# Kernel tuning notes

Measured on AMD Instinct MI355X. Metric: run time of the kernel, lower is better.

## Reference

```python
import jax, jax.numpy as jnp
import numpy as np

NUM_USERS = 100000
NUM_ITEMS = 50000
EMBED_DIM = 64
N_LAYERS = 3
NNZ = 4800000
BATCH = 16384
N_NODES = NUM_USERS + NUM_ITEMS


def setup_inputs() -> dict:
    key = jax.random.key(0)
    k1, k2, k3, k4, k5, k6, k7 = jax.random.split(key, 7)
    users = jax.random.randint(k1, (BATCH,), 0, NUM_USERS, dtype=jnp.int64 if jax.config.jax_enable_x64 else jnp.int32)
    items = jax.random.randint(k2, (BATCH,), 0, NUM_ITEMS, dtype=jnp.int64 if jax.config.jax_enable_x64 else jnp.int32)
    adj_rows = jax.random.randint(k3, (NNZ,), 0, N_NODES, dtype=jnp.int32)
    adj_cols = jax.random.randint(k4, (NNZ,), 0, N_NODES, dtype=jnp.int32)
    adj_vals = jax.random.uniform(k5, (NNZ,), dtype=jnp.float32)
    user_emb = jax.random.normal(k6, (NUM_USERS, EMBED_DIM), dtype=jnp.float32)
    item_emb = jax.random.normal(k7, (NUM_ITEMS, EMBED_DIM), dtype=jnp.float32)
    return {"users": users, "items": items, "adj_rows": adj_rows,
            "adj_cols": adj_cols, "adj_vals": adj_vals,
            "user_emb": user_emb, "item_emb": item_emb}


def _spmm(rows, cols, vals, x):
    # y = A @ x for COO sparse A: gather source rows, scale, scatter-add to dest
    return jax.ops.segment_sum(vals[:, None] * x[cols], rows, num_segments=N_NODES)


def reference(users, items, adj_rows, adj_cols, adj_vals, user_emb, item_emb):
    ego = jnp.concatenate([user_emb, item_emb], axis=0)  # [N_NODES, D]
    acc = ego
    cur = ego
    for _ in range(N_LAYERS):
        cur = _spmm(adj_rows, adj_cols, adj_vals, cur)
        acc = acc + cur
    mean_emb = acc / jnp.float32(N_LAYERS + 1)
    user_final = mean_emb[:NUM_USERS]
    item_final = mean_emb[NUM_USERS:]
    u = user_final[users]  # [B, D]
    i = item_final[items]  # [B, D]
    return jnp.sum(u * i, axis=-1)  # [B]
```

## Files before the change

### kernel.cpp

```cpp
#include <hip/hip_runtime.h>
#include <hip/hip_bf16.h>

#define NUM_USERS 100000
#define NUM_ITEMS 50000
#define EMBED_DIM 64
#define N_NODES   150000
#define ROW_SHIFT 9
#define ROWS_PER_BUCKET 512
#define B_BUCKETS ((N_NODES + ROWS_PER_BUCKET - 1) / ROWS_PER_BUCKET)
#define NBP 512
#define BIN_CHUNK 2048
#define COL_MASK 0x3FFFF

typedef unsigned short ushort_t;
typedef unsigned int uint_t;

__device__ __forceinline__ float bf16_to_f32(ushort_t u) {
    return __uint_as_float(((unsigned)u) << 16);
}
__device__ __forceinline__ ushort_t f32_to_bf16(float f) {
    return __builtin_bit_cast(ushort_t, __float2bfloat16(f));
}
__device__ __forceinline__ float bflo(uint_t r) {
    return __uint_as_float(r << 16);
}
__device__ __forceinline__ float bfhi(uint_t r) {
    return __uint_as_float(r & 0xffff0000u);
}

__global__ void __launch_bounds__(512) k_bucket_hist(const int* __restrict__ rows,
                                                     int* __restrict__ bhist, int nnz) {
    __shared__ int lh[NBP];
    int t = threadIdx.x;
    lh[t] = 0;
    __syncthreads();
    int base = blockIdx.x * (512 * 32);
#pragma unroll
    for (int k = 0; k < 32; k++) {
        int idx = base + k * 512 + t;
        if (idx < nnz) atomicAdd(&lh[rows[idx] >> ROW_SHIFT], 1);
    }
    __syncthreads();
    if (t < B_BUCKETS && lh[t] > 0) atomicAdd(&bhist[t], lh[t]);
}

__global__ void __launch_bounds__(512) k_bucket_scan(const int* __restrict__ bhist,
                                                     int* __restrict__ bucket_off,
                                                     int* __restrict__ bucket_cursor,
                                                     int* __restrict__ offs, int nnz) {
    __shared__ int lds[NBP];
    int t = threadIdx.x;
    int v = (t < B_BUCKETS) ? bhist[t] : 0;
    lds[t] = v;
    __syncthreads();
    for (int d = 1; d < NBP; d <<= 1) {
        int y = (t >= d) ? lds[t - d] : 0;
        __syncthreads();
        lds[t] += y;
        __syncthreads();
    }
    int excl = lds[t] - v;
    if (t < B_BUCKETS) {
        bucket_off[t] = excl;
        bucket_cursor[t] = excl;
    }
    if (t == 0) {
        bucket_off[B_BUCKETS] = nnz;
        offs[N_NODES] = nnz;
    }
}

__global__ void __launch_bounds__(512) k_bin(const int* __restrict__ rows,
                                             const int* __restrict__ cols,
                                             const float* __restrict__ vals,
                                             int* __restrict__ bucket_cursor,
                                             int2* __restrict__ staging, int nnz) {
    __shared__ int  ccnt[NBP];
    __shared__ int  cpos[NBP];
    __shared__ int  gdst[NBP];
    __shared__ int2 entries[BIN_CHUNK];
    __shared__ ushort_t ebuck[BIN_CHUNK];

    int t = threadIdx.x;
    int base = blockIdx.x * BIN_CHUNK;
    ccnt[t] = 0;
    __syncthreads();

    int myrow[BIN_CHUNK / 512];
#pragma unroll
    for (int k = 0; k < BIN_CHUNK / 512; k++) {
        int idx = base + k * 512 + t;
        int r = (idx < nnz) ? rows[idx] : -1;
        myrow[k] = r;
        if (r >= 0) atomicAdd(&ccnt[r >> ROW_SHIFT], 1);
    }
    __syncthreads();

    int c = ccnt[t];
    cpos[t] = c;
    __syncthreads();
    for (int d = 1; d < NBP; d <<= 1) {
        int y = (t >= d) ? cpos[t - d] : 0;
        __syncthreads();
        cpos[t] += y;
        __syncthreads();
    }
    int total = cpos[NBP - 1];
    int excl = cpos[t] - c;
    __syncthreads();
    cpos[t] = excl;
    __syncthreads();

#pragma unroll
    for (int k = 0; k < BIN_CHUNK / 512; k++) {
        int r = myrow[k];
        if (r >= 0) {
            int idx = base + k * 512 + t;
            int b = r >> ROW_SHIFT;
            int lrow = r & (ROWS_PER_BUCKET - 1);
            int slot = atomicAdd(&cpos[b], 1);
            entries[slot] = make_int2(cols[idx] | (lrow << 18), __float_as_int(vals[idx]));
            ebuck[slot] = (ushort_t)b;
        }
    }
    __syncthreads();

    if (t < B_BUCKETS && ccnt[t] > 0) {
        int g = atomicAdd(&bucket_cursor[t], ccnt[t]);
        gdst[t] = g - (cpos[t] - ccnt[t]);
    }
    __syncthreads();

    for (int i = t; i < total; i += 512) {
        staging[gdst[ebuck[i]] + i] = entries[i];
    }
}

__global__ void __launch_bounds__(512) k_scatter2(const int2* __restrict__ staging,
                                                  const int* __restrict__ bucket_off,
                                                  int* __restrict__ offs,
                                                  int2* __restrict__ cv) {
    __shared__ int rc[ROWS_PER_BUCKET];
    int b = blockIdx.x;
    int t = threadIdx.x;
    int beg = bucket_off[b], end = bucket_off[b + 1];
    int row0 = b << ROW_SHIFT;

    rc[t] = 0;
    __syncthreads();
    for (int i = beg + t; i < end; i += 512)
        atomicAdd(&rc[staging[i].x >> 18], 1);
    __syncthreads();

    int c = rc[t];
    for (int d = 1; d < ROWS_PER_BUCKET; d <<= 1) {
        int y = (t >= d) ? rc[t - d] : 0;
        __syncthreads();
        rc[t] += y;
        __syncthreads();
    }
    int excl = rc[t] - c;
    int row = row0 + t;
    if (row < N_NODES) offs[row] = beg + excl;
    __syncthreads();
    rc[t] = excl;
    __syncthreads();

    for (int i = beg + t; i < end; i += 512) {
        int2 e = staging[i];
        int pos = beg + atomicAdd(&rc[e.x >> 18], 1);
        cv[pos] = make_int2(e.x & COL_MASK, e.y);
    }
}

__global__ void k_convert(const float* __restrict__ ue, const float* __restrict__ ie,
                          ushort_t* __restrict__ xb) {
    int i = blockIdx.x * blockDim.x + threadIdx.x;
    const int n4 = (N_NODES * EMBED_DIM) / 4;
    if (i >= n4) return;
    const int usplit = (NUM_USERS * EMBED_DIM) / 4;
    float4 f = (i < usplit) ? ((const float4*)ue)[i] : ((const float4*)ie)[i - usplit];
    ushort4 o;
    o.x = f32_to_bf16(f.x);
    o.y = f32_to_bf16(f.y);
    o.z = f32_to_bf16(f.z);
    o.w = f32_to_bf16(f.w);
    ((ushort4*)xb)[i] = o;
}

__device__ __forceinline__ float2 spmm_row(int beg, int end, int hl, bool hi_half,
                                           const int2* __restrict__ cv,
                                           const ushort_t* __restrict__ xb) {
    const uint_t* __restrict__ xw = (const uint_t*)xb;
    float ax = 0.f, ay = 0.f;
    int e = beg;
    int npair = (end - beg) >> 1;
    int ng = npair >> 3;

    if (ng > 0) {
        uint_t r0[8], r1[8];
        float ve0[8], vo0[8], ve1[8], vo1[8];
#pragma unroll
        for (int j = 0; j < 8; j++) {
            int2 c0 = cv[e + 2 * j];
            int2 c1 = cv[e + 2 * j + 1];
            int ce = __builtin_amdgcn_readfirstlane(c0.x);
            int co = __builtin_amdgcn_readfirstlane(c1.x);
            ve0[j] = __int_as_float(__builtin_amdgcn_readfirstlane(c0.y));
            vo0[j] = __int_as_float(__builtin_amdgcn_readfirstlane(c1.y));
            int col = hi_half ? co : ce;
            r0[j] = xw[(size_t)col * 32 + hl];
        }
        e += 16;
#pragma unroll 1
        for (int g = 1; g < ng; g++) {
#pragma unroll
            for (int j = 0; j < 8; j++) {
                int2 c0 = cv[e + 2 * j];
                int2 c1 = cv[e + 2 * j + 1];
                int ce = __builtin_amdgcn_readfirstlane(c0.x);
                int co = __builtin_amdgcn_readfirstlane(c1.x);
                ve1[j] = __int_as_float(__builtin_amdgcn_readfirstlane(c0.y));
                vo1[j] = __int_as_float(__builtin_amdgcn_readfirstlane(c1.y));
                int col = hi_half ? co : ce;
                r1[j] = xw[(size_t)col * 32 + hl];
            }
            e += 16;
#pragma unroll
            for (int j = 0; j < 8; j++) {
                float v = hi_half ? vo0[j] : ve0[j];
                ax += v * bflo(r0[j]);
                ay += v * bfhi(r0[j]);
            }
#pragma unroll
            for (int j = 0; j < 8; j++) {
                r0[j] = r1[j]; ve0[j] = ve1[j]; vo0[j] = vo1[j];
            }
        }
#pragma unroll
        for (int j = 0; j < 8; j++) {
            float v = hi_half ? vo0[j] : ve0[j];
            ax += v * bflo(r0[j]);
            ay += v * bfhi(r0[j]);
        }
    }
#pragma unroll 1
    for (; e + 2 <= end; e += 2) {
        int2 c0 = cv[e];
        int2 c1 = cv[e + 1];
        int ce = __builtin_amdgcn_readfirstlane(c0.x);
        int co = __builtin_amdgcn_readfirstlane(c1.x);
        float ve = __int_as_float(__builtin_amdgcn_readfirstlane(c0.y));
        float vo = __int_as_float(__builtin_amdgcn_readfirstlane(c1.y));
        int col = hi_half ? co : ce;
        uint_t r = xw[(size_t)col * 32 + hl];
        float v = hi_half ? vo : ve;
        ax += v * bflo(r);
        ay += v * bfhi(r);
    }
    if (e < end) {
        int2 c = cv[e];
        int ce = __builtin_amdgcn_readfirstlane(c.x);
        float ve = __int_as_float(__builtin_amdgcn_readfirstlane(c.y));
        uint_t r = xw[(size_t)ce * 32 + hl];
        float v = hi_half ? 0.f : ve;
        ax += v * bflo(r);
        ay += v * bfhi(r);
    }
    ax += __shfl_xor(ax, 32, 64);
    ay += __shfl_xor(ay, 32, 64);
    return make_float2(ax, ay);
}

__global__ void k_spmm(const int* __restrict__ offs, const int2* __restrict__ cv,
                       const ushort_t* __restrict__ xb, ushort_t* __restrict__ out) {
    int row = (blockIdx.x * blockDim.x + threadIdx.x) >> 6;
    int lane = threadIdx.x & 63;
    if (row >= N_NODES) return;
    int hl = lane & 31;
    bool hi_half = lane >= 32;
    row = __builtin_amdgcn_readfirstlane(row);
    int beg = __builtin_amdgcn_readfirstlane(offs[row]);
    int end = __builtin_amdgcn_readfirstlane(offs[row + 1]);
    float2 a = spmm_row(beg, end, hl, hi_half, cv, xb);
    if (!hi_half) {
        uint_t packed = ((uint_t)f32_to_bf16(a.y) << 16) | (uint_t)f32_to_bf16(a.x);
        ((uint_t*)out)[(size_t)row * 32 + hl] = packed;
    }
}

__global__ void k_spmm_batch(const int* __restrict__ offs, const int2* __restrict__ cv,
                             const ushort_t* __restrict__ xb,
                             const int* __restrict__ users, const int* __restrict__ items,
                             float* __restrict__ u_acc, float* __restrict__ i_acc,
                             int batch) {
    int w = (blockIdx.x * blockDim.x + threadIdx.x) >> 6;
    int lane = threadIdx.x & 63;
    if (w >= 2 * batch) return;
    int hl = lane & 31;
    bool hi_half = lane >= 32;
    int b, row;
    float* dst;
    if (w < batch) { b = w;         row = users[b];             dst = u_acc; }
    else           { b = w - batch; row = NUM_USERS + items[b]; dst = i_acc; }
    row = __builtin_amdgcn_readfirstlane(row);
    int beg = __builtin_amdgcn_readfirstlane(offs[row]);
    int end = __builtin_amdgcn_readfirstlane(offs[row + 1]);
    float2 a = spmm_row(beg, end, hl, hi_half, cv, xb);
    if (!hi_half) {
        float2* d = (float2*)(dst + (size_t)b * EMBED_DIM) + hl;
        float2 cur = *d;
        cur.x += a.x;
        cur.y += a.y;
        *d = cur;
    }
}

__global__ void k_gather_f32(const int* __restrict__ users, const int* __restrict__ items,
                             const float* __restrict__ ue, const float* __restrict__ ie,
                             float* __restrict__ u_acc, float* __restrict__ i_acc, int batch) {
    int w = (blockIdx.x * blockDim.x + threadIdx.x) >> 6;
    int lane = threadIdx.x & 63;
    if (w >= batch) return;
    int nu = users[w];
    int ni = items[w];
    size_t o = (size_t)w * EMBED_DIM + lane;
    u_acc[o] = ue[(size_t)nu * EMBED_DIM + lane];
    i_acc[o] = ie[(size_t)ni * EMBED_DIM + lane];
}

__global__ void k_gather_bf16(const int* __restrict__ users, const int* __restrict__ items,
                              const ushort_t* __restrict__ xb,
                              float* __restrict__ u_acc, float* __restrict__ i_acc, int batch) {
    int w = (blockIdx.x * blockDim.x + threadIdx.x) >> 6;
    int lane = threadIdx.x & 63;
    if (w >= batch) return;
    int nu = users[w];
    int ni = NUM_USERS + items[w];
    size_t o = (size_t)w * EMBED_DIM + lane;
    u_acc[o] += bf16_to_f32(xb[(size_t)nu * EMBED_DIM + lane]);
    i_acc[o] += bf16_to_f32(xb[(size_t)ni * EMBED_DIM + lane]);
}

__global__ void k_dot(const float* __restrict__ u_acc, const float* __restrict__ i_acc,
                      float* __restrict__ out, int batch) {
    int w = (blockIdx.x * blockDim.x + threadIdx.x) >> 6;
    int lane = threadIdx.x & 63;
    if (w >= batch) return;
    size_t o = (size_t)w * EMBED_DIM + lane;
    float p = u_acc[o] * i_acc[o];
#pragma unroll
    for (int d = 32; d > 0; d >>= 1) p += __shfl_down(p, d, 64);
    if (lane == 0) out[w] = p * (1.0f / 16.0f);
}


extern "C" void kernel_launch(void* const* d_in, const int* in_sizes, int n_in,
                              void* d_out, int out_size, void* d_ws, size_t ws_size,
                              hipStream_t stream) {
    const int*   users    = (const int*)  d_in[0];
    const int*   items    = (const int*)  d_in[1];
    const int*   adj_rows = (const int*)  d_in[2];
    const int*   adj_cols = (const int*)  d_in[3];
    const float* adj_vals = (const float*)d_in[4];
    const float* user_emb = (const float*)d_in[5];
    const float* item_emb = (const float*)d_in[6];
    float* out = (float*)d_out;

    const int batch = in_sizes[0];
    const int nnz   = in_sizes[2];

    char* p = (char*)d_ws;
    auto alloc = [&](size_t bytes) -> char* {
        char* r = p;
        p += (bytes + 255) & ~(size_t)255;
        return r;
    };
    const size_t xb_bytes = (size_t)N_NODES * EMBED_DIM * 2;
    int*      offs          = (int*)  alloc(((size_t)N_NODES + 1) * 4);
    int*      bhist         = (int*)  alloc(NBP * 4);
    int*      bucket_off    = (int*)  alloc((NBP + 1) * 4);
    int*      bucket_cursor = (int*)  alloc(NBP * 4);
    int2*     cv            = (int2*) alloc((size_t)nnz * 8);
    size_t    region_bytes  = (size_t)nnz * 8;
    if (region_bytes < 2 * xb_bytes) region_bytes = 2 * xb_bytes;
    char*     region        = alloc(region_bytes);
    int2*     staging       = (int2*)region;
    ushort_t* xbA           = (ushort_t*)region;
    ushort_t* xbB           = (ushort_t*)(region + xb_bytes);
    ushort_t* xb_ego        = (ushort_t*)alloc(xb_bytes);
    float*    u_acc         = (float*)alloc((size_t)batch * EMBED_DIM * 4);
    float*    i_acc         = (float*)alloc((size_t)batch * EMBED_DIM * 4);

    const int g_bhist  = (nnz + 512 * 32 - 1) / (512 * 32);
    const int g_bin    = (nnz + BIN_CHUNK - 1) / BIN_CHUNK;
    const int g_conv   = ((N_NODES * EMBED_DIM / 4) + 255) / 256;
    const int g_nodes  = (N_NODES + 3) / 4;
    const int g_batch  = (batch + 3) / 4;
    const int g_batch2 = (2 * batch + 3) / 4;

    hipMemsetAsync(bhist, 0, NBP * 4, stream);
    k_bucket_hist<<<g_bhist, 512, 0, stream>>>(adj_rows, bhist, nnz);
    k_bucket_scan<<<1, 512, 0, stream>>>(bhist, bucket_off, bucket_cursor, offs, nnz);
    k_bin<<<g_bin, 512, 0, stream>>>(adj_rows, adj_cols, adj_vals, bucket_cursor, staging, nnz);
    k_scatter2<<<B_BUCKETS, 512, 0, stream>>>(staging, bucket_off, offs, cv);

    k_convert<<<g_conv, 256, 0, stream>>>(user_emb, item_emb, xb_ego);

    k_gather_f32<<<g_batch, 256, 0, stream>>>(users, items, user_emb, item_emb,
                                              u_acc, i_acc, batch);

    k_spmm<<<g_nodes, 256, 0, stream>>>(offs, cv, xb_ego, xbA);
    k_gather_bf16<<<g_batch, 256, 0, stream>>>(users, items, xbA, u_acc, i_acc, batch);

    k_spmm<<<g_nodes, 256, 0, stream>>>(offs, cv, xbA, xbB);
    k_gather_bf16<<<g_batch, 256, 0, stream>>>(users, items, xbB, u_acc, i_acc, batch);

    k_spmm_batch<<<g_batch2, 256, 0, stream>>>(offs, cv, xbB, users, items,
                                               u_acc, i_acc, batch);

    k_dot<<<g_batch, 256, 0, stream>>>(u_acc, i_acc, out, batch);
}
```

Baseline: 490.5 us.

## Fuse convert with histogram and fold per-layer gathers into final dot kernel

Merges the bf16 conversion of embeddings and the row-bucket histogram into one launch by splitting the grid between the two roles. Removes the per-layer gather/accumulate kernels and the separate dot kernel: the final kernel reads the ego, layer-1, layer-2 and layer-3 rows directly and computes the dot product. The spmm software pipeline is unrolled by two to swap register arrays instead of copying them. This reduces launch count and accumulator read-modify-write traffic. In exchange, the final kernel does more scattered reads.

```diff
diff --git a/kernel.cpp b/kernel.cpp
--- a/kernel.cpp
+++ b/kernel.cpp
@@ -11,6 +11,7 @@
 #define NBP 512
 #define BIN_CHUNK 2048
 #define COL_MASK 0x3FFFF
+#define PREP_HIST_CHUNK (256 * 64)
 
 typedef unsigned short ushort_t;
 typedef unsigned int uint_t;
@@ -28,20 +29,41 @@
     return __uint_as_float(r & 0xffff0000u);
 }
 
-__global__ void __launch_bounds__(512) k_bucket_hist(const int* __restrict__ rows,
-                                                     int* __restrict__ bhist, int nnz) {
-    __shared__ int lh[NBP];
+__global__ void __launch_bounds__(256) k_prep(const float* __restrict__ ue,
+                                              const float* __restrict__ ie,
+                                              ushort_t* __restrict__ xb,
+                                              const int* __restrict__ rows,
+                                              int* __restrict__ bhist,
+                                              int nnz, int g_conv) {
     int t = threadIdx.x;
-    lh[t] = 0;
-    __syncthreads();
-    int base = blockIdx.x * (512 * 32);
+    if ((int)blockIdx.x < g_conv) {
+        int i = blockIdx.x * 256 + t;
+        const int n4 = (N_NODES * EMBED_DIM) / 4;
+        if (i >= n4) return;
+        const int usplit = (NUM_USERS * EMBED_DIM) / 4;
+        float4 f = (i < usplit) ? ((const float4*)ue)[i] : ((const float4*)ie)[i - usplit];
+        ushort4 o;
+        o.x = f32_to_bf16(f.x);
+        o.y = f32_to_bf16(f.y);
+        o.z = f32_to_bf16(f.z);
+        o.w = f32_to_bf16(f.w);
+        ((ushort4*)xb)[i] = o;
+    } else {
+        __shared__ int lh[NBP];
+        lh[t] = 0;
+        lh[t + 256] = 0;
+        __syncthreads();
+        int bb = blockIdx.x - g_conv;
+        int base = bb * PREP_HIST_CHUNK;
 #pragma unroll
-    for (int k = 0; k < 32; k++) {
-        int idx = base + k * 512 + t;
-        if (idx < nnz) atomicAdd(&lh[rows[idx] >> ROW_SHIFT], 1);
-    }
-    __syncthreads();
-    if (t < B_BUCKETS && lh[t] > 0) atomicAdd(&bhist[t], lh[t]);
+        for (int k = 0; k < 64; k++) {
+            int idx = base + k * 256 + t;
+            if (idx < nnz) atomicAdd(&lh[rows[idx] >> ROW_SHIFT], 1);
+        }
+        __syncthreads();
+        for (int s = t; s < B_BUCKETS; s += 256)
+            if (lh[s] > 0) atomicAdd(&bhist[s], lh[s]);
+    }
 }
 
 __global__ void __launch_bounds__(512) k_bucket_scan(const int* __restrict__ bhist,
@@ -173,20 +195,27 @@
     }
 }
 
-__global__ void k_convert(const float* __restrict__ ue, const float* __restrict__ ie,
-                          ushort_t* __restrict__ xb) {
-    int i = blockIdx.x * blockDim.x + threadIdx.x;
-    const int n4 = (N_NODES * EMBED_DIM) / 4;
-    if (i >= n4) return;
-    const int usplit = (NUM_USERS * EMBED_DIM) / 4;
-    float4 f = (i < usplit) ? ((const float4*)ue)[i] : ((const float4*)ie)[i - usplit];
-    ushort4 o;
-    o.x = f32_to_bf16(f.x);
-    o.y = f32_to_bf16(f.y);
-    o.z = f32_to_bf16(f.z);
-    o.w = f32_to_bf16(f.w);
-    ((ushort4*)xb)[i] = o;
-}
+#define SPMM_LOAD(R, VE, VO)                                                  \
+    _Pragma("unroll")                                                         \
+    for (int j = 0; j < 8; j++) {                                             \
+        int2 c0 = cv[e + 2 * j];                                              \
+        int2 c1 = cv[e + 2 * j + 1];                                          \
+        int ce = __builtin_amdgcn_readfirstlane(c0.x);                        \
+        int co = __builtin_amdgcn_readfirstlane(c1.x);                        \
+        VE[j] = __int_as_float(__builtin_amdgcn_readfirstlane(c0.y));         \
+        VO[j] = __int_as_float(__builtin_amdgcn_readfirstlane(c1.y));         \
+        int col = hi_half ? co : ce;                                          \
+        R[j] = xw[(size_t)col * 32 + hl];                                     \
+    }                                                                         \
+    e += 16;
+
+#define SPMM_CONSUME(R, VE, VO)                                               \
+    _Pragma("unroll")                                                         \
+    for (int j = 0; j < 8; j++) {                                             \
+        float v = hi_half ? VO[j] : VE[j];                                    \
+        ax += v * bflo(R[j]);                                                 \
+        ay += v * bfhi(R[j]);                                                 \
+    }
 
 __device__ __forceinline__ float2 spmm_row(int beg, int end, int hl, bool hi_half,
                                            const int2* __restrict__ cv,
@@ -200,48 +229,21 @@
     if (ng > 0) {
         uint_t r0[8], r1[8];
         float ve0[8], vo0[8], ve1[8], vo1[8];
-#pragma unroll
-        for (int j = 0; j < 8; j++) {
-            int2 c0 = cv[e + 2 * j];
-            int2 c1 = cv[e + 2 * j + 1];
-            int ce = __builtin_amdgcn_readfirstlane(c0.x);
-            int co = __builtin_amdgcn_readfirstlane(c1.x);
-            ve0[j] = __int_as_float(__builtin_amdgcn_readfirstlane(c0.y));
-            vo0[j] = __int_as_float(__builtin_amdgcn_readfirstlane(c1.y));
-            int col = hi_half ? co : ce;
-            r0[j] = xw[(size_t)col * 32 + hl];
+        SPMM_LOAD(r0, ve0, vo0)
+        int g = 1;
+#pragma unroll 1
+        for (; g + 1 < ng; g += 2) {
+            SPMM_LOAD(r1, ve1, vo1)
+            SPMM_CONSUME(r0, ve0, vo0)
+            SPMM_LOAD(r0, ve0, vo0)
+            SPMM_CONSUME(r1, ve1, vo1)
         }
-        e += 16;
-#pragma unroll 1
-        for (int g = 1; g < ng; g++) {
-#pragma unroll
-            for (int j = 0; j < 8; j++) {
-                int2 c0 = cv[e + 2 * j];
-                int2 c1 = cv[e + 2 * j + 1];
-                int ce = __builtin_amdgcn_readfirstlane(c0.x);
-                int co = __builtin_amdgcn_readfirstlane(c1.x);
-                ve1[j] = __int_as_float(__builtin_amdgcn_readfirstlane(c0.y));
-                vo1[j] = __int_as_float(__builtin_amdgcn_readfirstlane(c1.y));
-                int col = hi_half ? co : ce;
-                r1[j] = xw[(size_t)col * 32 + hl];
-            }
-            e += 16;
-#pragma unroll
-            for (int j = 0; j < 8; j++) {
-                float v = hi_half ? vo0[j] : ve0[j];
-                ax += v * bflo(r0[j]);
-                ay += v * bfhi(r0[j]);
-            }
-#pragma unroll
-            for (int j = 0; j < 8; j++) {
-                r0[j] = r1[j]; ve0[j] = ve1[j]; vo0[j] = vo1[j];
-            }
-        }
-#pragma unroll
-        for (int j = 0; j < 8; j++) {
-            float v = hi_half ? vo0[j] : ve0[j];
-            ax += v * bflo(r0[j]);
-            ay += v * bfhi(r0[j]);
+        if (g < ng) {
+            SPMM_LOAD(r1, ve1, vo1)
+            SPMM_CONSUME(r0, ve0, vo0)
+            SPMM_CONSUME(r1, ve1, vo1)
+        } else {
+            SPMM_CONSUME(r0, ve0, vo0)
         }
     }
 #pragma unroll 1
@@ -292,7 +294,7 @@
 __global__ void k_spmm_batch(const int* __restrict__ offs, const int2* __restrict__ cv,
                              const ushort_t* __restrict__ xb,
                              const int* __restrict__ users, const int* __restrict__ items,
-                             float* __restrict__ u_acc, float* __restrict__ i_acc,
+                             float* __restrict__ u3, float* __restrict__ i3,
                              int batch) {
     int w = (blockIdx.x * blockDim.x + threadIdx.x) >> 6;
     int lane = threadIdx.x & 63;
@@ -301,54 +303,37 @@
     bool hi_half = lane >= 32;
     int b, row;
     float* dst;
-    if (w < batch) { b = w;         row = users[b];             dst = u_acc; }
-    else           { b = w - batch; row = NUM_USERS + items[b]; dst = i_acc; }
+    if (w < batch) { b = w;         row = users[b];             dst = u3; }
+    else           { b = w - batch; row = NUM_USERS + items[b]; dst = i3; }
     row = __builtin_amdgcn_readfirstlane(row);
     int beg = __builtin_amdgcn_readfirstlane(offs[row]);
     int end = __builtin_amdgcn_readfirstlane(offs[row + 1]);
     float2 a = spmm_row(beg, end, hl, hi_half, cv, xb);
     if (!hi_half) {
-        float2* d = (float2*)(dst + (size_t)b * EMBED_DIM) + hl;
-        float2 cur = *d;
-        cur.x += a.x;
-        cur.y += a.y;
-        *d = cur;
-    }
-}
-
-__global__ void k_gather_f32(const int* __restrict__ users, const int* __restrict__ items,
-                             const float* __restrict__ ue, const float* __restrict__ ie,
-                             float* __restrict__ u_acc, float* __restrict__ i_acc, int batch) {
+        ((float2*)(dst + (size_t)b * EMBED_DIM))[hl] = make_float2(a.x, a.y);
+    }
+}
+
+__global__ void k_final(const int* __restrict__ users, const int* __restrict__ items,
+                        const float* __restrict__ ue, const float* __restrict__ ie,
+                        const ushort_t* __restrict__ xbA, const ushort_t* __restrict__ xbB,
+                        const float* __restrict__ u3, const float* __restrict__ i3,
+                        float* __restrict__ out, int batch) {
     int w = (blockIdx.x * blockDim.x + threadIdx.x) >> 6;
     int lane = threadIdx.x & 63;
     if (w >= batch) return;
-    int nu = users[w];
-    int ni = items[w];
+    int uu = users[w];
+    int ii = items[w];
+    int nu = uu;
+    int ni = NUM_USERS + ii;
     size_t o = (size_t)w * EMBED_DIM + lane;
-    u_acc[o] = ue[(size_t)nu * EMBED_DIM + lane];
-    i_acc[o] = ie[(size_t)ni * EMBED_DIM + lane];
-}
-
-__global__ void k_gather_bf16(const int* __restrict__ users, const int* __restrict__ items,
-                              const ushort_t* __restrict__ xb,
-                              float* __restrict__ u_acc, float* __restrict__ i_acc, int batch) {
-    int w = (blockIdx.x * blockDim.x + threadIdx.x) >> 6;
-    int lane = threadIdx.x & 63;
-    if (w >= batch) return;
-    int nu = users[w];
-    int ni = NUM_USERS + items[w];
-    size_t o = (size_t)w * EMBED_DIM + lane;
-    u_acc[o] += bf16_to_f32(xb[(size_t)nu * EMBED_DIM + lane]);
-    i_acc[o] += bf16_to_f32(xb[(size_t)ni * EMBED_DIM + lane]);
-}
-
-__global__ void k_dot(const float* __restrict__ u_acc, const float* __restrict__ i_acc,
-                      float* __restrict__ out, int batch) {
-    int w = (blockIdx.x * blockDim.x + threadIdx.x) >> 6;
-    int lane = threadIdx.x & 63;
-    if (w >= batch) return;
-    size_t o = (size_t)w * EMBED_DIM + lane;
-    float p = u_acc[o] * i_acc[o];
+    size_t ou = (size_t)nu * EMBED_DIM + lane;
+    size_t oi = (size_t)ni * EMBED_DIM + lane;
+    float u = ue[(size_t)uu * EMBED_DIM + lane]
+            + bf16_to_f32(xbA[ou]) + bf16_to_f32(xbB[ou]) + u3[o];
+    float i = ie[(size_t)ii * EMBED_DIM + lane]
+            + bf16_to_f32(xbA[oi]) + bf16_to_f32(xbB[oi]) + i3[o];
+    float p = u * i;
 #pragma unroll
     for (int d = 32; d > 0; d >>= 1) p += __shfl_down(p, d, 64);
     if (lane == 0) out[w] = p * (1.0f / 16.0f);
@@ -389,35 +374,30 @@
     ushort_t* xbA           = (ushort_t*)region;
     ushort_t* xbB           = (ushort_t*)(region + xb_bytes);
     ushort_t* xb_ego        = (ushort_t*)alloc(xb_bytes);
-    float*    u_acc         = (float*)alloc((size_t)batch * EMBED_DIM * 4);
-    float*    i_acc         = (float*)alloc((size_t)batch * EMBED_DIM * 4);
-
-    const int g_bhist  = (nnz + 512 * 32 - 1) / (512 * 32);
+    float*    u3            = (float*)alloc((size_t)batch * EMBED_DIM * 4);
+    float*    i3            = (float*)alloc((size_t)batch * EMBED_DIM * 4);
+
+    const int g_conv   = ((N_NODES * EMBED_DIM / 4) + 255) / 256;
+    const int g_hist   = (nnz + PREP_HIST_CHUNK - 1) / PREP_HIST_CHUNK;
     const int g_bin    = (nnz + BIN_CHUNK - 1) / BIN_CHUNK;
-    const int g_conv   = ((N_NODES * EMBED_DIM / 4) + 255) / 256;
     const int g_nodes  = (N_NODES + 3) / 4;
     const int g_batch  = (batch + 3) / 4;
     const int g_batch2 = (2 * batch + 3) / 4;
 
     hipMemsetAsync(bhist, 0, NBP * 4, stream);
-    k_bucket_hist<<<g_bhist, 512, 0, stream>>>(adj_rows, bhist, nnz);
+    k_prep<<<g_conv + g_hist, 256, 0, stream>>>(user_emb, item_emb, xb_ego,
+                                                adj_rows, bhist, nnz, g_conv);
     k_bucket_scan<<<1, 512, 0, stream>>>(bhist, bucket_off, bucket_cursor, offs, nnz);
     k_bin<<<g_bin, 512, 0, stream>>>(adj_rows, adj_cols, adj_vals, bucket_cursor, staging, nnz);
     k_scatter2<<<B_BUCKETS, 512, 0, stream>>>(staging, bucket_off, offs, cv);
 
-    k_convert<<<g_conv, 256, 0, stream>>>(user_emb, item_emb, xb_ego);
-
-    k_gather_f32<<<g_batch, 256, 0, stream>>>(users, items, user_emb, item_emb,
-                                              u_acc, i_acc, batch);
-
     k_spmm<<<g_nodes, 256, 0, stream>>>(offs, cv, xb_ego, xbA);
-    k_gather_bf16<<<g_batch, 256, 0, stream>>>(users, items, xbA, u_acc, i_acc, batch);
 
     k_spmm<<<g_nodes, 256, 0, stream>>>(offs, cv, xbA, xbB);
-    k_gather_bf16<<<g_batch, 256, 0, stream>>>(users, items, xbB, u_acc, i_acc, batch);
 
     k_spmm_batch<<<g_batch2, 256, 0, stream>>>(offs, cv, xbB, users, items,
-                                               u_acc, i_acc, batch);
-
-    k_dot<<<g_batch, 256, 0, stream>>>(u_acc, i_acc, out, batch);
-}
+                                               u3, i3, batch);
+
+    k_final<<<g_batch, 256, 0, stream>>>(users, items, user_emb, item_emb,
+                                         xbA, xbB, u3, i3, out, batch);
+}
```

Result: no change. 481.6 us (-1.8%).
